# Optimization experiments

Measured on AMD Instinct MI355X. Metric: run time of the kernel, lower is better.

Reference implementation:

```python
import jax, jax.numpy as jnp
import numpy as np

D_IN = 4096
NUM_HEADS = 32
HEAD_DIM = 128
NUM_KV = 8
GROUP = NUM_HEADS // NUM_KV
EPS = 1e-6
ROPE_BASE = 10000.0


def rms_norm(x, scale):
    # norm over last dim (head_dim), computed in fp32 as in torch ref
    var = jnp.mean(x * x, axis=-1, keepdims=True)
    return x * jax.lax.rsqrt(var + EPS) * scale


def rope_cos_sin(positions, dim):
    inv_freq = 1.0 / (ROPE_BASE ** (jnp.arange(0, dim, 2, dtype=jnp.float32) / dim))
    angles = positions.astype(jnp.float32)[:, None] * inv_freq[None, :]  # (N, dim/2)
    angles = jnp.concatenate([angles, angles], axis=-1)  # (N, dim)
    return jnp.cos(angles), jnp.sin(angles)


def apply_rope(t, cos, sin):
    # t: (N, heads, D); cos/sin: (N, D)
    half = t.shape[-1] // 2
    rot = jnp.concatenate([-t[..., half:], t[..., :half]], axis=-1)
    return t * cos[:, None, :] + rot * sin[:, None, :]


def setup_inputs() -> dict:
    key = jax.random.key(0)
    ks = jax.random.split(key, 6)
    B, S = 1, 2048
    x = jax.random.normal(ks[0], (B, S, D_IN), dtype=jnp.float32)
    positions = jnp.arange(B * S, dtype=jnp.int32)
    sc = 0.02
    Wq = jax.random.normal(ks[1], (D_IN, NUM_HEADS * HEAD_DIM), dtype=jnp.float32) * sc
    Wk = jax.random.normal(ks[2], (D_IN, NUM_KV * HEAD_DIM), dtype=jnp.float32) * sc
    Wv = jax.random.normal(ks[3], (D_IN, NUM_KV * HEAD_DIM), dtype=jnp.float32) * sc
    Wo = jax.random.normal(ks[4], (NUM_HEADS * HEAD_DIM, D_IN), dtype=jnp.float32) * sc
    q_scale = jnp.ones((HEAD_DIM,), dtype=jnp.float32)
    k_scale = jnp.ones((HEAD_DIM,), dtype=jnp.float32)
    return {"x": x, "positions": positions, "Wq": Wq, "Wk": Wk, "Wv": Wv,
            "Wo": Wo, "q_scale": q_scale, "k_scale": k_scale}


def reference(x, positions, Wq, Wk, Wv, Wo, q_scale, k_scale):
    B, S, _ = x.shape
    N = B * S
    xf = x.reshape(N, D_IN)
    q = (xf @ Wq).reshape(N, NUM_HEADS, HEAD_DIM)
    k = (xf @ Wk).reshape(N, NUM_KV, HEAD_DIM)
    v = (xf @ Wv).reshape(N, NUM_KV, HEAD_DIM)
    # QK RMSNorm over head_dim
    q = rms_norm(q, q_scale)
    k = rms_norm(k, k_scale)
    # RoPE (rotate-half)
    cos, sin = rope_cos_sin(positions, HEAD_DIM)
    q = apply_rope(q, cos, sin)
    k = apply_rope(k, cos, sin)
    # (B, KV, group, S, D) for q; (B, KV, S, D) for k, v  (GQA broadcast)
    q = q.reshape(B, S, NUM_KV, GROUP, HEAD_DIM).transpose(0, 2, 3, 1, 4)
    k = k.reshape(B, S, NUM_KV, HEAD_DIM).transpose(0, 2, 1, 3)
    v = v.reshape(B, S, NUM_KV, HEAD_DIM).transpose(0, 2, 1, 3)
    scale = 1.0 / jnp.sqrt(jnp.float32(HEAD_DIM))
    scores = jnp.einsum('bghsd,bgtd->bghst', q, k) * scale  # (B,KV,G,S,S)
    causal = jnp.tril(jnp.ones((S, S), dtype=bool))
    scores = jnp.where(causal[None, None, None, :, :], scores, jnp.finfo(scores.dtype).min)
    attn = jax.nn.softmax(scores, axis=-1)
    ctx = jnp.einsum('bghst,bgtd->bghsd', attn, v)  # (B,KV,G,S,D)
    ctx = ctx.transpose(0, 3, 1, 2, 4).reshape(B, S, NUM_HEADS * HEAD_DIM)
    return ctx @ Wo
```

## Files before the change

### kernel.cpp

```cpp
#include <hip/hip_runtime.h>

#define S_LEN 2048
#define DMODEL 4096
#define NQKV 6144

typedef unsigned short u16;
typedef __attribute__((ext_vector_type(8))) short bf16x8;
typedef __attribute__((ext_vector_type(8))) unsigned short u16x8;
typedef __attribute__((ext_vector_type(4))) float f32x4;

#define NEG_BIG (-3.0e38f)

__device__ __forceinline__ float bf2f(u16 h) {
    union { unsigned u; float f; } c; c.u = ((unsigned)h) << 16; return c.f;
}
__device__ __forceinline__ u16 f2bf(float x) {
    union { float f; unsigned u; } c; c.f = x;
    return (u16)((c.u + 0x7fffu + ((c.u >> 16) & 1u)) >> 16);
}

__device__ __forceinline__ void gload16(const void* g, void* l) {
    __builtin_amdgcn_global_load_lds(
        (const __attribute__((address_space(1))) void*)g,
        (__attribute__((address_space(3))) void*)l, 16, 0, 0);
}

__device__ __forceinline__ void barfence() {
    asm volatile("" ::: "memory");
    __builtin_amdgcn_s_barrier();
    asm volatile("" ::: "memory");
}

#define MFMA16(d, av, bv) d = __builtin_amdgcn_mfma_f32_16x16x32_bf16(av, bv, d, 0, 0, 0)

__global__ __launch_bounds__(256) void detect_dtype(const u16* __restrict__ probe,
                                                    int* __restrict__ flags) {
    __shared__ int bad_s;
    if (threadIdx.x == 0) bad_s = 0;
    __syncthreads();
    int bad = 0;
    for (int i = threadIdx.x; i < 16384; i += 256) {
        float v = bf2f(probe[i]);
        if (!(fabsf(v) < 1e6f)) bad = 1;
    }
    if (bad) atomicOr(&bad_s, 1);
    __syncthreads();
    if (threadIdx.x == 0) { flags[0] = bad_s; flags[1] = 0; }
}

__global__ __launch_bounds__(256) void conv_bf16(const void* __restrict__ src,
                                                 u16* __restrict__ dst, long n,
                                                 const int* __restrict__ flag) {
    const bool f32 = (*flag != 0);
    long i = (long)blockIdx.x * 256 + threadIdx.x;
    long stride = (long)gridDim.x * 256;
    for (; i < n; i += stride) {
        float v = f32 ? ((const float*)src)[i] : bf2f(((const u16*)src)[i]);
        dst[i] = f2bf(v);
    }
}

__global__ __launch_bounds__(256) void transpose_any(
        const void* __restrict__ src, long base_off, long sld, long szoff,
        u16* __restrict__ dst, long dld, long dzoff,
        const int* __restrict__ flag) {
    __shared__ alignas(16) u16 tile[32][33];
    const bool f32 = (*flag != 0);
    u16* d = dst + (long)blockIdx.z * dzoff;
    long soff = base_off + (long)blockIdx.z * szoff;
    int c0 = blockIdx.x * 32, r0 = blockIdx.y * 32;
    int tx = threadIdx.x & 31, ty = threadIdx.x >> 5;
    for (int i = 0; i < 32; i += 8) {
        long idx = soff + (long)(r0 + ty + i) * sld + c0 + tx;
        float v = f32 ? ((const float*)src)[idx] : bf2f(((const u16*)src)[idx]);
        tile[ty + i][tx] = f2bf(v);
    }
    __syncthreads();
    for (int i = 0; i < 32; i += 8)
        d[(long)(c0 + ty + i) * dld + r0 + tx] = tile[tx][ty + i];
}

__device__ __forceinline__ void st_out(u16* C, size_t idx, float v)   { C[idx] = f2bf(v); }
__device__ __forceinline__ void st_out(float* C, size_t idx, float v) { C[idx] = v; }

template <typename OUT>
__device__ __forceinline__ void gemm_dp2_core(
        const u16* __restrict__ A, const u16* __restrict__ BT,
        OUT* __restrict__ C, int K, int ldc) {
    __shared__ alignas(16) u16 smem[65536];
    const int tid = threadIdx.x;
    const int lane = tid & 63, wid = tid >> 6;
    const int wr = wid >> 2, wc = wid & 3;
    const int lm = lane & 15, lq = lane >> 4;
    const int m0 = blockIdx.y * 256, n0 = blockIdx.x * 256;

    const int srow = tid >> 3;
    const int sgrp = (tid & 7) ^ (srow & 7);
    const u16* aS = A  + (size_t)(m0 + srow) * K + sgrp * 8;
    const u16* bS = BT + (size_t)(n0 + srow) * K + sgrp * 8;
    u16* ldsA = smem + tid * 8;
    u16* ldsB = smem + 16384 + tid * 8;

    auto stA = [&](int bufi, int c, int kti) {
        gload16(aS + (size_t)c * 64 * K + (size_t)kti * 64, ldsA + bufi * 32768 + c * 4096);
    };
    auto stB = [&](int bufi, int c, int kti) {
        gload16(bS + (size_t)c * 64 * K + (size_t)kti * 64, ldsB + bufi * 32768 + c * 4096);
    };
    auto rdA = [&](const u16* buf, int mi, int ks) {
        int row = wr * 128 + mi * 16 + lm;
        return *(const bf16x8*)(const void*)(buf + row * 64 + (((ks * 4 + lq) ^ (row & 7)) << 3));
    };
    auto rdB = [&](const u16* buf, int ni, int ks) {
        int row = wc * 64 + ni * 16 + lm;
        return *(const bf16x8*)(const void*)(buf + 16384 + row * 64 + (((ks * 4 + lq) ^ (row & 7)) << 3));
    };

    const int NK = K >> 6;
    stB(0, 0, 0); stB(0, 1, 0); stB(0, 2, 0); stB(0, 3, 0);
    stA(0, 0, 0); stA(0, 2, 0); stA(0, 1, 0); stA(0, 3, 0);

    f32x4 acc[8][4] = {};
    bf16x8 b[4][2], a[2][2];

#pragma unroll 2
    for (int kt = 0; kt < NK; ++kt) {
        const u16* buf = smem + (kt & 1) * 32768;
        const int nb = (kt & 1) ^ 1;
        const int kn = kt + 1;
        const bool more = kn < NK;

        asm volatile("s_waitcnt vmcnt(2)" ::: "memory");
        barfence();
#pragma unroll
        for (int ni = 0; ni < 4; ++ni)
#pragma unroll
            for (int ks = 0; ks < 2; ++ks) b[ni][ks] = rdB(buf, ni, ks);
#pragma unroll
        for (int q = 0; q < 2; ++q)
#pragma unroll
            for (int ks = 0; ks < 2; ++ks) a[q][ks] = rdA(buf, q, ks);
        if (more) { stB(nb, 0, kn); stB(nb, 1, kn); }
        __builtin_amdgcn_s_setprio(1);
#pragma unroll
        for (int q = 0; q < 2; ++q)
#pragma unroll
            for (int ni = 0; ni < 4; ++ni)
#pragma unroll
                for (int ks = 0; ks < 2; ++ks) MFMA16(acc[q][ni], a[q][ks], b[ni][ks]);
        __builtin_amdgcn_s_setprio(0);

#pragma unroll
        for (int q = 0; q < 2; ++q)
#pragma unroll
            for (int ks = 0; ks < 2; ++ks) a[q][ks] = rdA(buf, 2 + q, ks);
        if (more) { stB(nb, 2, kn); stB(nb, 3, kn); }
        __builtin_amdgcn_s_setprio(1);
#pragma unroll
        for (int q = 0; q < 2; ++q)
#pragma unroll
            for (int ni = 0; ni < 4; ++ni)
#pragma unroll
                for (int ks = 0; ks < 2; ++ks) MFMA16(acc[2 + q][ni], a[q][ks], b[ni][ks]);
        __builtin_amdgcn_s_setprio(0);

        if (more) { asm volatile("s_waitcnt vmcnt(4)" ::: "memory"); }
        else      { asm volatile("s_waitcnt vmcnt(0)" ::: "memory"); }
        barfence();
#pragma unroll
        for (int q = 0; q < 2; ++q)
#pragma unroll
            for (int ks = 0; ks < 2; ++ks) a[q][ks] = rdA(buf, 4 + q, ks);
        if (more) { stA(nb, 0, kn); stA(nb, 2, kn); }
        __builtin_amdgcn_s_setprio(1);
#pragma unroll
        for (int q = 0; q < 2; ++q)
#pragma unroll
            for (int ni = 0; ni < 4; ++ni)
#pragma unroll
                for (int ks = 0; ks < 2; ++ks) MFMA16(acc[4 + q][ni], a[q][ks], b[ni][ks]);
        __builtin_amdgcn_s_setprio(0);

#pragma unroll
        for (int q = 0; q < 2; ++q)
#pragma unroll
            for (int ks = 0; ks < 2; ++ks) a[q][ks] = rdA(buf, 6 + q, ks);
        if (more) { stA(nb, 1, kn); stA(nb, 3, kn); }
        __builtin_amdgcn_s_setprio(1);
#pragma unroll
        for (int q = 0; q < 2; ++q)
#pragma unroll
            for (int ni = 0; ni < 4; ++ni)
#pragma unroll
                for (int ks = 0; ks < 2; ++ks) MFMA16(acc[6 + q][ni], a[q][ks], b[ni][ks]);
        __builtin_amdgcn_s_setprio(0);
    }

#pragma unroll
    for (int mi = 0; mi < 8; ++mi)
#pragma unroll
        for (int ni = 0; ni < 4; ++ni) {
            int col  = n0 + wc * 64 + ni * 16 + lm;
            int rowb = m0 + wr * 128 + mi * 16 + lq * 4;
#pragma unroll
            for (int r = 0; r < 4; ++r)
                st_out(C, (size_t)(rowb + r) * ldc + col, acc[mi][ni][r]);
        }
}

__global__ __launch_bounds__(512, 2) void gemm_dp2_bf16(
        const u16* __restrict__ A, const u16* __restrict__ BT,
        u16* __restrict__ C, int K, int ldc) {
    gemm_dp2_core<u16>(A, BT, C, K, ldc);
}
__global__ __launch_bounds__(512, 2) void gemm_dp2_f32(
        const u16* __restrict__ A, const u16* __restrict__ BT,
        float* __restrict__ C, int K, int ldc) {
    gemm_dp2_core<float>(A, BT, C, K, ldc);
}

__global__ __launch_bounds__(256) void rms_rope(
        const u16* __restrict__ qkv, const int* __restrict__ pos,
        const u16* __restrict__ qs, const u16* __restrict__ kscale,
        u16* __restrict__ Qb, u16* __restrict__ Kb) {
    int w = threadIdx.x >> 6, lane = threadIdx.x & 63;
    int task = blockIdx.x * 4 + w;
    int h = task >> 11, row = task & 2047;
    int base = (h < 32) ? h * 128 : 4096 + (h - 32) * 128;
    const u16* src = qkv + (size_t)row * NQKV + base;
    float t0 = bf2f(src[lane]), t1 = bf2f(src[lane + 64]);
    float ss = t0 * t0 + t1 * t1;
    for (int m = 1; m < 64; m <<= 1) ss += __shfl_xor(ss, m);
    float inv = rsqrtf(ss * (1.0f / 128.0f) + 1e-6f);
    const u16* sc = (h < 32) ? qs : kscale;
    float n0 = t0 * inv * bf2f(sc[lane]);
    float n1 = t1 * inv * bf2f(sc[lane + 64]);
    float p = (float)pos[row];
    float ang = p * __expf(-(float)lane * (9.210340371976184f / 64.0f));
    float c = cosf(ang), s = sinf(ang);
    float o0 = n0 * c - n1 * s;
    float o1 = n1 * c + n0 * s;
    float mul = (h < 32) ? 0.08838834764831845f : 1.0f;
    u16* dst = (h < 32) ? (Qb + ((size_t)h * S_LEN + row) * 128)
                        : (Kb + ((size_t)(h - 32) * S_LEN + row) * 128);
    dst[lane] = f2bf(o0 * mul);
    dst[lane + 64] = f2bf(o1 * mul);
}

__global__ __launch_bounds__(256, 2) void flash_attn(
        const u16* __restrict__ Qb, const u16* __restrict__ Kb,
        const u16* __restrict__ VTb, u16* __restrict__ ctx) {
    const int h = blockIdx.y, kvh = h >> 2;
    const int tid = threadIdx.x, lane = tid & 63, w = tid >> 6;
    const int lm = lane & 15, lq = lane >> 4;
    const int swz = (lm & 7) << 3;
    __shared__ alignas(16) u16 smem[20480];
    u16* Ksm = smem;
    u16* Vsm = smem + 8192;
    u16* Psm = smem + 16384;
    const u16* Kh = Kb + (size_t)kvh * S_LEN * 128;
    const u16* Vh = VTb + (size_t)kvh * 128 * S_LEN;

    for (int pass = 0; pass < 2; ++pass) {
        const int t = pass ? (31 - blockIdx.x) : blockIdx.x;
        const u16* Qh = Qb + ((size_t)h * S_LEN + (size_t)t * 64) * 128;

        __syncthreads();
        for (int i = 0; i < 4; ++i) {
            int g = i * 256 + tid;
            int row = g >> 4, s = g & 15;
            int sp = (s & 8) | ((s ^ row) & 7);
            gload16(Qh + (size_t)row * 128 + sp * 8,
                    Ksm + (size_t)(i * 256 + w * 64) * 8);
        }
        __syncthreads();
        bf16x8 aq[4];
        for (int ks = 0; ks < 4; ++ks)
            aq[ks] = *(const bf16x8*)(const void*)(
                Ksm + (((w * 16 + lm) * 128 + ks * 32 + lq * 8) ^ swz));

        float mrow[4], lrow[4];
        f32x4 accO[8];
        const f32x4 zero = {0.f, 0.f, 0.f, 0.f};
        for (int r = 0; r < 4; ++r) { mrow[r] = NEG_BIG; lrow[r] = 0.f; }
        for (int di = 0; di < 8; ++di) accO[di] = zero;

        for (int j = 0; j <= t; ++j) {
            __syncthreads();
            for (int i = 0; i < 4; ++i) {
                int g = i * 256 + tid;
                int row = g >> 4, s = g & 15;
                int sp = (s & 8) | ((s ^ row) & 7);
                gload16(Kh + (size_t)(j * 64 + row) * 128 + sp * 8,
                        Ksm + (size_t)(i * 256 + w * 64) * 8);
            }
            for (int i = 0; i < 4; ++i) {
                int g = i * 256 + tid;
                int d = g >> 3, s = g & 7;
                int sp = s ^ (d & 7);
                gload16(Vh + (size_t)d * S_LEN + j * 64 + sp * 8,
                        Vsm + (size_t)(i * 256 + w * 64) * 8);
            }
            __syncthreads();

            f32x4 sacc[4] = {};
            for (int ks = 0; ks < 4; ++ks) {
                bf16x8 kf[4];
                for (int ni = 0; ni < 4; ++ni)
                    kf[ni] = *(const bf16x8*)(const void*)(
                        Ksm + (((ni * 16 + lm) * 128 + ks * 32 + lq * 8) ^ swz));
                for (int ni = 0; ni < 4; ++ni)
                    sacc[ni] = __builtin_amdgcn_mfma_f32_16x16x32_bf16(aq[ks], kf[ni], sacc[ni], 0, 0, 0);
            }

            if (j == t) {
                for (int ni = 0; ni < 4; ++ni) {
                    int col = ni * 16 + lm;
                    for (int r = 0; r < 4; ++r)
                        if (col > w * 16 + lq * 4 + r) sacc[ni][r] = NEG_BIG;
                }
            }

            for (int r = 0; r < 4; ++r) {
                float mx = fmaxf(fmaxf(sacc[0][r], sacc[1][r]),
                                 fmaxf(sacc[2][r], sacc[3][r]));
                for (int sft = 1; sft < 16; sft <<= 1) mx = fmaxf(mx, __shfl_xor(mx, sft));
                float mN = fmaxf(mrow[r], mx);
                float alpha = __expf(mrow[r] - mN);
                mrow[r] = mN;
                float psum = 0.f;
                int prow = w * 16 + lq * 4 + r;
                for (int ni = 0; ni < 4; ++ni) {
                    float pv = __expf(sacc[ni][r] - mN);
                    psum += pv;
                    Psm[prow * 64 + ((ni * 16 + lm) ^ ((prow & 7) << 3))] = f2bf(pv);
                }
                for (int sft = 1; sft < 16; sft <<= 1) psum += __shfl_xor(psum, sft);
                lrow[r] = lrow[r] * alpha + psum;
                for (int di = 0; di < 8; ++di) accO[di][r] *= alpha;
            }
            __syncthreads();

            for (int ks2 = 0; ks2 < 2; ++ks2) {
                bf16x8 pf = *(const bf16x8*)(const void*)(
                    Psm + (((w * 16 + lm) * 64 + ks2 * 32 + lq * 8) ^ swz));
                for (int di = 0; di < 8; ++di) {
                    bf16x8 vf = *(const bf16x8*)(const void*)(
                        Vsm + (((di * 16 + lm) * 64 + ks2 * 32 + lq * 8) ^ swz));
                    accO[di] = __builtin_amdgcn_mfma_f32_16x16x32_bf16(pf, vf, accO[di], 0, 0, 0);
                }
            }
        }

        for (int r = 0; r < 4; ++r) {
            float invl = 1.0f / fmaxf(lrow[r], 1e-30f);
            size_t rowg = (size_t)t * 64 + w * 16 + lq * 4 + r;
            for (int di = 0; di < 8; ++di)
                ctx[rowg * 4096 + h * 128 + di * 16 + lm] = f2bf(accO[di][r] * invl);
        }
    }
}

extern "C" void kernel_launch(void* const* d_in, const int* in_sizes, int n_in,
                              void* d_out, int out_size, void* d_ws, size_t ws_size,
                              hipStream_t stream) {
    const void* x   = d_in[0];
    const int* pos  = (const int*)d_in[1];
    const void* Wq  = d_in[2];
    const void* Wk  = d_in[3];
    const void* Wv  = d_in[4];
    const void* Wo  = d_in[5];
    const void* qs  = d_in[6];
    const void* ks  = d_in[7];

    if (ws_size < (size_t)145 * 1024 * 1024) return;
    char* ws = (char*)d_ws;
    u16* WqkvT = (u16*)ws;
    u16* WoT   = (u16*)(ws + (size_t)48  * 1024 * 1024);
    u16* qkv   = (u16*)(ws + (size_t)80  * 1024 * 1024);
    u16* ctx   = qkv;
    u16* Qb    = (u16*)(ws + (size_t)104 * 1024 * 1024);
    u16* Kb    = (u16*)(ws + (size_t)120 * 1024 * 1024);
    u16* VTb   = (u16*)(ws + (size_t)124 * 1024 * 1024);
    u16* xb    = (u16*)(ws + (size_t)128 * 1024 * 1024);
    int* flags = (int*)(ws + (size_t)144 * 1024 * 1024);
    u16* qsb   = (u16*)(ws + (size_t)144 * 1024 * 1024 + 1024);
    u16* ksb   = (u16*)(ws + (size_t)144 * 1024 * 1024 + 2048);

    dim3 b256(256);
    const int* flag  = flags;
    const int* fzero = flags + 1;

    detect_dtype<<<1, b256, 0, stream>>>((const u16*)Wq, flags);
    conv_bf16<<<8192, b256, 0, stream>>>(x,  xb,  (long)S_LEN * DMODEL, flag);
    conv_bf16<<<1,    b256, 0, stream>>>(qs, qsb, 128, flag);
    conv_bf16<<<1,    b256, 0, stream>>>(ks, ksb, 128, flag);

    transpose_any<<<dim3(128, 128, 1), b256, 0, stream>>>(Wq, 0, 4096, 0, WqkvT, 4096, 0, flag);
    transpose_any<<<dim3(32, 128, 1),  b256, 0, stream>>>(Wk, 0, 1024, 0, WqkvT + (size_t)4096 * 4096, 4096, 0, flag);
    transpose_any<<<dim3(32, 128, 1),  b256, 0, stream>>>(Wv, 0, 1024, 0, WqkvT + (size_t)5120 * 4096, 4096, 0, flag);
    transpose_any<<<dim3(128, 128, 1), b256, 0, stream>>>(Wo, 0, 4096, 0, WoT, 4096, 0, flag);

    gemm_dp2_bf16<<<dim3(24, 8), dim3(512), 0, stream>>>(xb, WqkvT, qkv, 4096, NQKV);
    rms_rope<<<dim3(20480), b256, 0, stream>>>(qkv, pos, qsb, ksb, Qb, Kb);
    transpose_any<<<dim3(4, 64, 8), b256, 0, stream>>>(qkv, 5120, NQKV, 128, VTb, 2048, (long)128 * 2048, fzero);
    flash_attn<<<dim3(16, 32), b256, 0, stream>>>(Qb, Kb, VTb, ctx);
    gemm_dp2_f32<<<dim3(16, 8), dim3(512), 0, stream>>>(ctx, WoT, (float*)d_out, 4096, 4096);
}
```

Measured before the change: 561.4 us.

## Double-buffer K/V tiles in flash attention and retile output projection GEMM

Flash attention now prefetches the next K/V tile into a second LDS buffer while computing the current one. It uses explicit vmcnt waits and barrier fences instead of full syncthreads. The output projection GEMM is replaced with a new 128x256-tile kernel that double-buffers its loads, launched on a 16x16 grid so more blocks fill the CUs. The cost is extra LDS use per attention block, which could lower occupancy, and finer waitcnt bookkeeping that is easy to get wrong.

```diff
diff --git a/kernel.cpp b/kernel.cpp
--- a/kernel.cpp
+++ b/kernel.cpp
@@ -213,10 +213,101 @@
         u16* __restrict__ C, int K, int ldc) {
     gemm_dp2_core<u16>(A, BT, C, K, ldc);
 }
-__global__ __launch_bounds__(512, 2) void gemm_dp2_f32(
+
+__global__ __launch_bounds__(512, 2) void gemm_dp3_f32(
         const u16* __restrict__ A, const u16* __restrict__ BT,
         float* __restrict__ C, int K, int ldc) {
-    gemm_dp2_core<float>(A, BT, C, K, ldc);
+    __shared__ alignas(16) u16 smem[49152];
+    const int tid = threadIdx.x;
+    const int lane = tid & 63, wid = tid >> 6;
+    const int wr = wid >> 1, wc = wid & 1;
+    const int lm = lane & 15, lq = lane >> 4;
+    const int m0 = blockIdx.y * 128, n0 = blockIdx.x * 256;
+
+    const int srow = tid >> 3;
+    const int sgrp = (tid & 7) ^ (srow & 7);
+    const u16* aS = A  + (size_t)(m0 + srow) * K + sgrp * 8;
+    const u16* bS = BT + (size_t)(n0 + srow) * K + sgrp * 8;
+    u16* ldsA = smem + tid * 8;
+    u16* ldsB = smem + 8192 + tid * 8;
+
+    auto stA = [&](int bufi, int c, int kti) {
+        gload16(aS + (size_t)c * 64 * K + (size_t)kti * 64, ldsA + bufi * 24576 + c * 4096);
+    };
+    auto stB = [&](int bufi, int c, int kti) {
+        gload16(bS + (size_t)c * 64 * K + (size_t)kti * 64, ldsB + bufi * 24576 + c * 4096);
+    };
+    auto rdA = [&](const u16* buf, int mi, int ks) {
+        int row = wr * 32 + mi * 16 + lm;
+        return *(const bf16x8*)(const void*)(buf + row * 64 + (((ks * 4 + lq) ^ (row & 7)) << 3));
+    };
+    auto rdB = [&](const u16* buf, int ni, int ks) {
+        int row = wc * 128 + ni * 16 + lm;
+        return *(const bf16x8*)(const void*)(buf + 8192 + row * 64 + (((ks * 4 + lq) ^ (row & 7)) << 3));
+    };
+
+    const int NK = K >> 6;
+    stA(0, 0, 0); stA(0, 1, 0); stB(0, 0, 0); stB(0, 2, 0);
+    stB(0, 1, 0); stB(0, 3, 0);
+
+    f32x4 acc[2][8] = {};
+    bf16x8 a[2][2], b[4][2];
+
+#pragma unroll 2
+    for (int kt = 0; kt < NK; ++kt) {
+        const u16* buf = smem + (kt & 1) * 24576;
+        const int nb = (kt & 1) ^ 1;
+        const int kn = kt + 1;
+        const bool more = kn < NK;
+
+        asm volatile("s_waitcnt vmcnt(2)" ::: "memory");
+        barfence();
+#pragma unroll
+        for (int mi = 0; mi < 2; ++mi)
+#pragma unroll
+            for (int ks = 0; ks < 2; ++ks) a[mi][ks] = rdA(buf, mi, ks);
+#pragma unroll
+        for (int ni = 0; ni < 4; ++ni)
+#pragma unroll
+            for (int ks = 0; ks < 2; ++ks) b[ni][ks] = rdB(buf, ni, ks);
+        if (more) { stA(nb, 0, kn); stA(nb, 1, kn); stB(nb, 0, kn); stB(nb, 2, kn); }
+        __builtin_amdgcn_s_setprio(1);
+#pragma unroll
+        for (int mi = 0; mi < 2; ++mi)
+#pragma unroll
+            for (int ni = 0; ni < 4; ++ni)
+#pragma unroll
+                for (int ks = 0; ks < 2; ++ks) MFMA16(acc[mi][ni], a[mi][ks], b[ni][ks]);
+        __builtin_amdgcn_s_setprio(0);
+
+        if (more) { asm volatile("s_waitcnt vmcnt(4)" ::: "memory"); }
+        else      { asm volatile("s_waitcnt vmcnt(0)" ::: "memory"); }
+        barfence();
+#pragma unroll
+        for (int ni = 0; ni < 4; ++ni)
+#pragma unroll
+            for (int ks = 0; ks < 2; ++ks) b[ni][ks] = rdB(buf, 4 + ni, ks);
+        if (more) { stB(nb, 1, kn); stB(nb, 3, kn); }
+        __builtin_amdgcn_s_setprio(1);
+#pragma unroll
+        for (int mi = 0; mi < 2; ++mi)
+#pragma unroll
+            for (int ni = 0; ni < 4; ++ni)
+#pragma unroll
+                for (int ks = 0; ks < 2; ++ks) MFMA16(acc[mi][4 + ni], a[mi][ks], b[ni][ks]);
+        __builtin_amdgcn_s_setprio(0);
+    }
+
+#pragma unroll
+    for (int mi = 0; mi < 2; ++mi)
+#pragma unroll
+        for (int ni = 0; ni < 8; ++ni) {
+            int col  = n0 + wc * 128 + ni * 16 + lm;
+            int rowb = m0 + wr * 32 + mi * 16 + lq * 4;
+#pragma unroll
+            for (int r = 0; r < 4; ++r)
+                C[(size_t)(rowb + r) * ldc + col] = acc[mi][ni][r];
+        }
 }
 
 __global__ __launch_bounds__(256) void rms_rope(
@@ -254,30 +345,51 @@
     const int tid = threadIdx.x, lane = tid & 63, w = tid >> 6;
     const int lm = lane & 15, lq = lane >> 4;
     const int swz = (lm & 7) << 3;
-    __shared__ alignas(16) u16 smem[20480];
-    u16* Ksm = smem;
-    u16* Vsm = smem + 8192;
-    u16* Psm = smem + 16384;
+    __shared__ alignas(16) u16 smem[36864];
+    u16* Psm = smem + 32768;
     const u16* Kh = Kb + (size_t)kvh * S_LEN * 128;
     const u16* Vh = VTb + (size_t)kvh * 128 * S_LEN;
+
+    auto stageK = [&](int j) {
+        for (int i = 0; i < 4; ++i) {
+            int g = i * 256 + tid;
+            int row = g >> 4, s = g & 15;
+            int sp = (s & 8) | ((s ^ row) & 7);
+            gload16(Kh + (size_t)(j * 64 + row) * 128 + sp * 8,
+                    smem + (j & 1) * 8192 + (size_t)(i * 256 + w * 64) * 8);
+        }
+    };
+    auto stageV = [&](int j) {
+        for (int i = 0; i < 4; ++i) {
+            int g = i * 256 + tid;
+            int d = g >> 3, s = g & 7;
+            int sp = s ^ (d & 7);
+            gload16(Vh + (size_t)d * S_LEN + j * 64 + sp * 8,
+                    smem + 16384 + (j & 1) * 8192 + (size_t)(i * 256 + w * 64) * 8);
+        }
+    };
 
     for (int pass = 0; pass < 2; ++pass) {
         const int t = pass ? (31 - blockIdx.x) : blockIdx.x;
         const u16* Qh = Qb + ((size_t)h * S_LEN + (size_t)t * 64) * 128;
 
-        __syncthreads();
+        barfence();
         for (int i = 0; i < 4; ++i) {
             int g = i * 256 + tid;
             int row = g >> 4, s = g & 15;
             int sp = (s & 8) | ((s ^ row) & 7);
             gload16(Qh + (size_t)row * 128 + sp * 8,
-                    Ksm + (size_t)(i * 256 + w * 64) * 8);
-        }
-        __syncthreads();
+                    smem + (size_t)(i * 256 + w * 64) * 8);
+        }
+        asm volatile("s_waitcnt vmcnt(0)" ::: "memory");
+        barfence();
         bf16x8 aq[4];
         for (int ks = 0; ks < 4; ++ks)
             aq[ks] = *(const bf16x8*)(const void*)(
-                Ksm + (((w * 16 + lm) * 128 + ks * 32 + lq * 8) ^ swz));
+                smem + (((w * 16 + lm) * 128 + ks * 32 + lq * 8) ^ swz));
+        asm volatile("s_waitcnt lgkmcnt(0)" ::: "memory");
+        barfence();
+        stageK(0); stageV(0);
 
         float mrow[4], lrow[4];
         f32x4 accO[8];
@@ -286,29 +398,22 @@
         for (int di = 0; di < 8; ++di) accO[di] = zero;
 
         for (int j = 0; j <= t; ++j) {
-            __syncthreads();
-            for (int i = 0; i < 4; ++i) {
-                int g = i * 256 + tid;
-                int row = g >> 4, s = g & 15;
-                int sp = (s & 8) | ((s ^ row) & 7);
-                gload16(Kh + (size_t)(j * 64 + row) * 128 + sp * 8,
-                        Ksm + (size_t)(i * 256 + w * 64) * 8);
+            const u16* Kj = smem + (j & 1) * 8192;
+            const u16* Vj = smem + 16384 + (j & 1) * 8192;
+            if (j < t) {
+                stageK(j + 1); stageV(j + 1);
+                asm volatile("s_waitcnt vmcnt(8)" ::: "memory");
+            } else {
+                asm volatile("s_waitcnt vmcnt(0)" ::: "memory");
             }
-            for (int i = 0; i < 4; ++i) {
-                int g = i * 256 + tid;
-                int d = g >> 3, s = g & 7;
-                int sp = s ^ (d & 7);
-                gload16(Vh + (size_t)d * S_LEN + j * 64 + sp * 8,
-                        Vsm + (size_t)(i * 256 + w * 64) * 8);
-            }
-            __syncthreads();
+            barfence();
 
             f32x4 sacc[4] = {};
             for (int ks = 0; ks < 4; ++ks) {
                 bf16x8 kf[4];
                 for (int ni = 0; ni < 4; ++ni)
                     kf[ni] = *(const bf16x8*)(const void*)(
-                        Ksm + (((ni * 16 + lm) * 128 + ks * 32 + lq * 8) ^ swz));
+                        Kj + (((ni * 16 + lm) * 128 + ks * 32 + lq * 8) ^ swz));
                 for (int ni = 0; ni < 4; ++ni)
                     sacc[ni] = __builtin_amdgcn_mfma_f32_16x16x32_bf16(aq[ks], kf[ni], sacc[ni], 0, 0, 0);
             }
@@ -339,17 +444,19 @@
                 lrow[r] = lrow[r] * alpha + psum;
                 for (int di = 0; di < 8; ++di) accO[di][r] *= alpha;
             }
-            __syncthreads();
+            asm volatile("s_waitcnt lgkmcnt(0)" ::: "memory");
+            barfence();
 
             for (int ks2 = 0; ks2 < 2; ++ks2) {
                 bf16x8 pf = *(const bf16x8*)(const void*)(
                     Psm + (((w * 16 + lm) * 64 + ks2 * 32 + lq * 8) ^ swz));
                 for (int di = 0; di < 8; ++di) {
                     bf16x8 vf = *(const bf16x8*)(const void*)(
-                        Vsm + (((di * 16 + lm) * 64 + ks2 * 32 + lq * 8) ^ swz));
+                        Vj + (((di * 16 + lm) * 64 + ks2 * 32 + lq * 8) ^ swz));
                     accO[di] = __builtin_amdgcn_mfma_f32_16x16x32_bf16(pf, vf, accO[di], 0, 0, 0);
                 }
             }
+            barfence();
         }
 
         for (int r = 0; r < 4; ++r) {
@@ -405,5 +512,5 @@
     rms_rope<<<dim3(20480), b256, 0, stream>>>(qkv, pos, qsb, ksb, Qb, Kb);
     transpose_any<<<dim3(4, 64, 8), b256, 0, stream>>>(qkv, 5120, NQKV, 128, VTb, 2048, (long)128 * 2048, fzero);
     flash_attn<<<dim3(16, 32), b256, 0, stream>>>(Qb, Kb, VTb, ctx);
-    gemm_dp2_f32<<<dim3(16, 8), dim3(512), 0, stream>>>(ctx, WoT, (float*)d_out, 4096, 4096);
-}
+    gemm_dp3_f32<<<dim3(16, 16), dim3(512), 0, stream>>>(ctx, WoT, (float*)d_out, 4096, 4096);
+}
```

Result: faster. 534.0 us (-4.9%).
